# Kernel optimization log

Hardware: AMD Instinct MI355X
Metric: run time of the kernel (lower is better)

Reference implementation:

```python
import jax, jax.numpy as jnp
import numpy as np
from jax import lax

DWT_SCALE = 0.5
IDWT_SCALE = 1.0
PAD = 2  # (kernel_size-1)//2 for k=5


def haar_dwt(x, s):
    """x: [B,C,H,W] -> (ll, lh, hl, hh) each [B,C,H/2,W/2]. 2x2 Haar, scale s."""
    a = x[..., 0::2, 0::2]
    b = x[..., 0::2, 1::2]
    c = x[..., 1::2, 0::2]
    d = x[..., 1::2, 1::2]
    ll = s * (a + b + c + d)
    lh = s * (a + b - c - d)
    hl = s * (a - b + c - d)
    hh = s * (a - b - c + d)
    return ll, lh, hl, hh


def haar_idwt(ll, lh, hl, hh, s):
    """Inverse of haar_dwt when s_dwt * s_idwt_total = 0.5. Returns [B,C,2H,2W]."""
    a = s * (ll + lh + hl + hh)
    b = s * (ll + lh - hl - hh)
    c = s * (ll - lh + hl - hh)
    d = s * (ll - lh - hl + hh)
    B, C, H2, W2 = ll.shape
    top = jnp.stack([a, b], axis=-1).reshape(B, C, H2, 2 * W2)  # even rows
    bot = jnp.stack([c, d], axis=-1).reshape(B, C, H2, 2 * W2)  # odd rows
    return jnp.stack([top, bot], axis=-2).reshape(B, C, 2 * H2, 2 * W2)


def conv2d(x, w, pad):
    return lax.conv_general_dilated(
        x, w, window_strides=(1, 1), padding=[(pad, pad), (pad, pad)],
        dimension_numbers=("NCHW", "OIHW", "NCHW"))


def setup_inputs() -> dict:
    key = jax.random.key(0)
    kx, k0, k1, k2, kb = jax.random.split(key, 5)
    C, K = 64, 5
    x = jax.random.normal(kx, (8, C, 256, 256), dtype=jnp.float32)
    # kaiming_uniform-ish small init to keep 3-level recursion numerically tame
    scale = 0.02
    w0 = jax.random.normal(k0, (4 * C, 4 * C, K, K), dtype=jnp.float32) * scale
    w1 = jax.random.normal(k1, (4 * C, 4 * C, K, K), dtype=jnp.float32) * scale
    w2 = jax.random.normal(k2, (4 * C, 4 * C, K, K), dtype=jnp.float32) * scale
    bias = jax.random.normal(kb, (C,), dtype=jnp.float32) * 0.01
    return {"x": x, "w0": w0, "w1": w1, "w2": w2, "bias": bias}


def reference(x, w0, w1, w2, bias):
    weights = [w0, w1, w2]
    idwt_s = DWT_SCALE * IDWT_SCALE  # perfect reconstruction pair
    curr = x
    ll_levels, high_levels = [], []
    for w in weights:
        ll, lh, hl, hh = haar_dwt(curr, DWT_SCALE)
        curr = ll  # pre-conv LL feeds the next level
        B, C, H2, W2 = ll.shape
        stacked = jnp.stack([ll, lh, hl, hh], axis=2).reshape(B, 4 * C, H2, W2)
        y = conv2d(stacked, w, PAD)  # [B, 4*Co, H2, W2]
        y = y.reshape(B, -1, 4, H2, W2)
        ll_levels.append(y[:, :, 0])
        high_levels.append(y[:, :, 1:])
    next_ll = jnp.zeros_like(ll_levels[-1])
    for ll_t, h_t in zip(reversed(ll_levels), reversed(high_levels)):
        ll = ll_t + next_ll
        next_ll = haar_idwt(ll, h_t[:, :, 0], h_t[:, :, 1], h_t[:, :, 2], idwt_s)
    return next_ll + bias.reshape(1, -1, 1, 1)
```

## Files before the change

### kernel.cpp

```cpp
#include <hip/hip_runtime.h>


typedef unsigned short u16;
typedef __attribute__((ext_vector_type(8))) __bf16 bf16x8;
typedef __attribute__((ext_vector_type(4))) float f32x4;

__device__ __forceinline__ u16 f2bf(float f) {
  union { float f; unsigned u; } v; v.f = f;
  unsigned r = v.u + 0x7fffu + ((v.u >> 16) & 1u);
  return (u16)(r >> 16);
}
__device__ __forceinline__ float bf2f(u16 u) {
  union { unsigned u; float f; } v; v.u = ((unsigned)u) << 16;
  return v.f;
}

typedef const unsigned int __attribute__((address_space(1)))* gas1_t;
typedef unsigned int __attribute__((address_space(3)))* gas3_t;
__device__ __forceinline__ void gload16(const void* g, void* l) {
  __builtin_amdgcn_global_load_lds((gas1_t)g, (gas3_t)l, 16, 0, 0);
}

__global__ void k_wtrans(const float* __restrict__ w, u16* __restrict__ wb) {
  int co = blockIdx.x;
  int ci = threadIdx.x;
  const float* src = w + ((long)co * 256 + ci) * 25;
  float v[25];
#pragma unroll
  for (int tp = 0; tp < 25; ++tp) v[tp] = src[tp];
#pragma unroll
  for (int tp = 0; tp < 25; ++tp)
    wb[((long)tp * 256 + co) * 256 + ci] = f2bf(v[tp]);
}

__global__ void k_dwt(const float* __restrict__ in, u16* __restrict__ st,
                      float* __restrict__ ll, int B_, int H2, int W2) {
  int idx = blockIdx.x * blockDim.x + threadIdx.x;
  int W2h = W2 >> 1;
  int total = B_ * 64 * H2 * W2h;
  if (idx >= total) return;
  int w2h = idx % W2h; int t2 = idx / W2h;
  int h2 = t2 % H2; t2 /= H2;
  int c = t2 % 64; int b = t2 / 64;
  int w2 = w2h * 2;
  const float* r0 = in + (((long)(b * 64 + c) * (2 * H2) + 2 * h2) * (2 * W2)) + 2 * w2;
  const float* r1 = r0 + 2 * W2;
  float4 tp = *(const float4*)r0;
  float4 bt = *(const float4*)r1;
  float ll0 = 0.5f * (tp.x + tp.y + bt.x + bt.y);
  float lh0 = 0.5f * (tp.x + tp.y - bt.x - bt.y);
  float hl0 = 0.5f * (tp.x - tp.y + bt.x - bt.y);
  float hh0 = 0.5f * (tp.x - tp.y - bt.x + bt.y);
  float ll1 = 0.5f * (tp.z + tp.w + bt.z + bt.w);
  float lh1 = 0.5f * (tp.z + tp.w - bt.z - bt.w);
  float hl1 = 0.5f * (tp.z - tp.w + bt.z - bt.w);
  float hh1 = 0.5f * (tp.z - tp.w - bt.z + bt.w);
  long sbase = (((long)b * (H2 + 4) + (h2 + 2)) * (W2 + 4) + (w2 + 2)) * 256 + 4 * c;
  *(ushort4*)(st + sbase)       = make_ushort4(f2bf(ll0), f2bf(lh0), f2bf(hl0), f2bf(hh0));
  *(ushort4*)(st + sbase + 256) = make_ushort4(f2bf(ll1), f2bf(lh1), f2bf(hl1), f2bf(hh1));
  long lbase = (((long)(b * 64 + c) * H2) + h2) * W2 + w2;
  *(float2*)(ll + lbase) = make_float2(ll0, ll1);
}

__global__ __launch_bounds__(512, 1) void k_conv_p(
    const u16* __restrict__ st, const u16* __restrict__ wt, u16* __restrict__ y,
    int H2, int W2) {
  __shared__ __align__(16) char smem[147456];
  const int t = threadIdx.x;
  const int lane = t & 63;
  const int wv = t >> 6;
  const int wm = wv >> 2;
  const int wn = wv & 3;
  const int nwg = gridDim.x;
  const int bid = blockIdx.x;
  const int lb = (bid & 7) * (nwg >> 3) + (bid >> 3);
  const int m0 = lb * 128;
  const int PW = W2 + 4;

  const int trow = t >> 3;
  const int srcci = ((t & 7) ^ (trow & 7)) * 8;
  const char* baseA[2];
  const char* baseB[4];
#pragma unroll
  for (int h = 0; h < 2; ++h) {
    int m = m0 + h * 64 + trow;
    int w = m % W2; int q = m / W2;
    int hh = q % H2; int b = q / H2;
    long sp = ((long)(b * (H2 + 4) + hh + 2) * PW + (w + 2));
    baseA[h] = (const char*)(st + sp * 256 + srcci);
  }
#pragma unroll
  for (int u = 0; u < 4; ++u) {
    int n = u * 64 + trow;
    baseB[u] = (const char*)(wt + (long)n * 256 + srcci);
  }

  f32x4 acc[4][4];
#pragma unroll
  for (int i = 0; i < 4; ++i)
#pragma unroll
    for (int j = 0; j < 4; ++j) acc[i][j] = f32x4{0.f, 0.f, 0.f, 0.f};

  const int kq = (lane >> 4) * 16;
  int aoff[2][4], boff[2][4];
#pragma unroll
  for (int ks = 0; ks < 2; ++ks)
#pragma unroll
    for (int i = 0; i < 4; ++i) {
      int ra = wm * 64 + i * 16 + (lane & 15);
      int kb = ks * 64 + kq;
      aoff[ks][i] = ra * 128 + (kb ^ ((ra & 7) << 4));
      int rb = wn * 64 + i * 16 + (lane & 15);
      boff[ks][i] = 16384 + rb * 128 + (kb ^ ((rb & 7) << 4));
    }

  auto stage_a = [&](int kt) {
    int tap = kt >> 2, cic = kt & 3;
    int dy = tap / 5 - 2, dx = tap % 5 - 2;
    long offA = ((long)(dy * PW + dx) * 256 + cic * 64) * 2;
    long offB = ((long)tap * 65536 + cic * 64) * 2;
    char* lb2 = smem + (kt % 3) * 49152 + wv * 1024;
    gload16(baseA[0] + offA, lb2);
    gload16(baseA[1] + offA, lb2 + 8192);
    gload16(baseB[0] + offB, lb2 + 16384);
  };
  auto stage_b = [&](int kt) {
    int tap = kt >> 2, cic = kt & 3;
    long offB = ((long)tap * 65536 + cic * 64) * 2;
    char* lb2 = smem + (kt % 3) * 49152 + wv * 1024;
    gload16(baseB[1] + offB, lb2 + 24576);
    gload16(baseB[2] + offB, lb2 + 32768);
    gload16(baseB[3] + offB, lb2 + 40960);
  };

  stage_a(0); stage_b(0);
  stage_a(1); stage_b(1);
  asm volatile("s_waitcnt vmcnt(6)" ::: "memory");
  __builtin_amdgcn_s_barrier();

  for (int kt = 0; kt < 100; ++kt) {
    const char* la = smem + (kt % 3) * 49152;
    const bool st2 = (kt + 2) < 100;
    bf16x8 af[4], bfr[4];
#pragma unroll
    for (int i = 0; i < 4; ++i) af[i] = *(const bf16x8*)(la + aoff[0][i]);
#pragma unroll
    for (int j = 0; j < 4; ++j) bfr[j] = *(const bf16x8*)(la + boff[0][j]);
    if (st2) stage_a(kt + 2);
    __builtin_amdgcn_s_barrier();
    asm volatile("s_waitcnt lgkmcnt(0)" ::: "memory");
    __builtin_amdgcn_sched_barrier(0);
    __builtin_amdgcn_s_setprio(1);
#pragma unroll
    for (int i = 0; i < 4; ++i)
#pragma unroll
      for (int j = 0; j < 4; ++j)
        acc[i][j] = __builtin_amdgcn_mfma_f32_16x16x32_bf16(af[i], bfr[j], acc[i][j], 0, 0, 0);
    __builtin_amdgcn_s_setprio(0);
    __builtin_amdgcn_s_barrier();
#pragma unroll
    for (int i = 0; i < 4; ++i) af[i] = *(const bf16x8*)(la + aoff[1][i]);
#pragma unroll
    for (int j = 0; j < 4; ++j) bfr[j] = *(const bf16x8*)(la + boff[1][j]);
    if (st2) stage_b(kt + 2);
    __builtin_amdgcn_s_barrier();
    asm volatile("s_waitcnt lgkmcnt(0)" ::: "memory");
    __builtin_amdgcn_sched_barrier(0);
    __builtin_amdgcn_s_setprio(1);
#pragma unroll
    for (int i = 0; i < 4; ++i)
#pragma unroll
      for (int j = 0; j < 4; ++j)
        acc[i][j] = __builtin_amdgcn_mfma_f32_16x16x32_bf16(af[i], bfr[j], acc[i][j], 0, 0, 0);
    __builtin_amdgcn_s_setprio(0);
    if (st2) {
      asm volatile("s_waitcnt vmcnt(6)" ::: "memory");
    } else if (kt + 1 < 100) {
      asm volatile("s_waitcnt vmcnt(0)" ::: "memory");
    }
    __builtin_amdgcn_s_barrier();
  }

#pragma unroll
  for (int i = 0; i < 4; ++i) {
    int mloc = m0 + wm * 64 + i * 16 + (lane >> 4) * 4;
#pragma unroll
    for (int j = 0; j < 4; ++j) {
      int nloc = wn * 64 + j * 16 + (lane & 15);
#pragma unroll
      for (int r = 0; r < 4; ++r)
        y[(long)(mloc + r) * 256 + nloc] = f2bf(acc[i][j][r]);
    }
  }
}

__global__ __launch_bounds__(256) void k_conv(
    const u16* __restrict__ st, const u16* __restrict__ wt, u16* __restrict__ y,
    int H2, int W2) {
  __shared__ __align__(16) char smem[32768];
  const int t = threadIdx.x;
  const int lane = t & 63;
  const int wv = t >> 6;
  const int wm = wv >> 1, wn = wv & 1;
  const int m0 = blockIdx.x * 128;
  const int n0 = blockIdx.y * 128;
  const int PW = W2 + 4;
  const int lsub = lane & 7;
  const int lrow8 = lane >> 3;
  const int srcci = (lsub ^ lrow8) * 8;

  const char* baseA[4];
  const char* baseB[4];
#pragma unroll
  for (int l = 0; l < 4; ++l) {
    int ml = (wv * 4 + l) * 8 + lrow8;
    int m = m0 + ml;
    int w = m % W2;
    int q = m / W2;
    int h = q % H2;
    int b = q / H2;
    long sp = ((long)(b * (H2 + 4) + h + 2) * PW + (w + 2));
    baseA[l] = (const char*)(st + sp * 256 + srcci);
    int nl = n0 + (wv * 4 + l) * 8 + lrow8;
    baseB[l] = (const char*)(wt + (long)nl * 256 + srcci);
  }

  f32x4 acc[4][4];
#pragma unroll
  for (int i = 0; i < 4; ++i)
#pragma unroll
    for (int j = 0; j < 4; ++j) acc[i][j] = f32x4{0.f, 0.f, 0.f, 0.f};

  const int arow = wm * 64 + (lane & 15);
  const int brow = wn * 64 + (lane & 15);
  const int kq = (lane >> 4) * 16;
  int aoff[2][4], boff[2][4];
#pragma unroll
  for (int ks = 0; ks < 2; ++ks)
#pragma unroll
    for (int i = 0; i < 4; ++i) {
      int ra = arow + i * 16;
      int kb = ks * 64 + kq;
      aoff[ks][i] = ra * 128 + (kb ^ ((ra & 7) << 4));
      int rb = brow + i * 16;
      boff[ks][i] = 16384 + rb * 128 + (kb ^ ((rb & 7) << 4));
    }

  for (int kk = 0; kk < 100; ++kk) {
    const int tap = kk >> 2, cic = kk & 3;
    const int dy = tap / 5 - 2, dx = tap % 5 - 2;
    const int offA = ((dy * PW + dx) * 256 + cic * 64) * 2;
    const int offB = (tap * 65536 + cic * 64) * 2;
#pragma unroll
    for (int l = 0; l < 4; ++l) {
      gload16(baseA[l] + offA, smem + (wv * 4 + l) * 1024);
      gload16(baseB[l] + offB, smem + 16384 + (wv * 4 + l) * 1024);
    }
    __syncthreads();
#pragma unroll
    for (int ks = 0; ks < 2; ++ks) {
      bf16x8 af[4], bfr[4];
#pragma unroll
      for (int i = 0; i < 4; ++i) af[i] = *(const bf16x8*)(smem + aoff[ks][i]);
#pragma unroll
      for (int j = 0; j < 4; ++j) bfr[j] = *(const bf16x8*)(smem + boff[ks][j]);
#pragma unroll
      for (int i = 0; i < 4; ++i)
#pragma unroll
        for (int j = 0; j < 4; ++j)
          acc[i][j] = __builtin_amdgcn_mfma_f32_16x16x32_bf16(af[i], bfr[j], acc[i][j], 0, 0, 0);
    }
    __syncthreads();
  }

  const long ybase = (long)m0 * 256 + n0;
#pragma unroll
  for (int i = 0; i < 4; ++i) {
    int mloc = wm * 64 + i * 16 + (lane >> 4) * 4;
#pragma unroll
    for (int j = 0; j < 4; ++j) {
      int nloc = wn * 64 + j * 16 + (lane & 15);
#pragma unroll
      for (int r = 0; r < 4; ++r)
        y[ybase + (long)(mloc + r) * 256 + nloc] = f2bf(acc[i][j][r]);
    }
  }
}

__global__ void k_idwt(const u16* __restrict__ y, const float* __restrict__ nll,
                       float* __restrict__ out, const float* __restrict__ bias,
                       int B_, int H2, int W2) {
  int idx = blockIdx.x * blockDim.x + threadIdx.x;
  int W2h = W2 >> 1;
  int total = B_ * 64 * H2 * W2h;
  if (idx >= total) return;
  int w2h = idx % W2h; int t2 = idx / W2h;
  int h2 = t2 % H2; t2 /= H2;
  int c = t2 % 64; int b = t2 / 64;
  int w2 = w2h * 2;
  long ybase = (((long)b * H2 + h2) * W2 + w2) * 256 + 4 * c;
  ushort4 q0 = *(const ushort4*)(y + ybase);
  ushort4 q1 = *(const ushort4*)(y + ybase + 256);
  float llv0 = bf2f(q0.x), lh0 = bf2f(q0.y), hl0 = bf2f(q0.z), hh0 = bf2f(q0.w);
  float llv1 = bf2f(q1.x), lh1 = bf2f(q1.y), hl1 = bf2f(q1.z), hh1 = bf2f(q1.w);
  if (nll) {
    float2 nv = *(const float2*)(nll + (((long)(b * 64 + c) * H2 + h2) * W2 + w2));
    llv0 += nv.x; llv1 += nv.y;
  }
  float bv = bias ? bias[c] : 0.f;
  float a0 = 0.5f * (llv0 + lh0 + hl0 + hh0) + bv;
  float b0 = 0.5f * (llv0 + lh0 - hl0 - hh0) + bv;
  float c0 = 0.5f * (llv0 - lh0 + hl0 - hh0) + bv;
  float d0 = 0.5f * (llv0 - lh0 - hl0 + hh0) + bv;
  float a1 = 0.5f * (llv1 + lh1 + hl1 + hh1) + bv;
  float b1 = 0.5f * (llv1 + lh1 - hl1 - hh1) + bv;
  float c1 = 0.5f * (llv1 - lh1 + hl1 - hh1) + bv;
  float d1 = 0.5f * (llv1 - lh1 - hl1 + hh1) + bv;
  long obase = (((long)(b * 64 + c) * (2 * H2) + 2 * h2) * (2 * W2)) + 2 * w2;
  *(float4*)(out + obase)             = make_float4(a0, b0, a1, b1);
  *(float4*)(out + obase + 2 * W2)    = make_float4(c0, d0, c1, d1);
}

constexpr size_t WBF_SZ1 = 25ull * 256 * 256 * 2;
constexpr size_t OFF_WBF = 0;
constexpr size_t OFF_S0  = 3 * WBF_SZ1;
constexpr size_t S0_SZ   = 8ull * 132 * 132 * 256 * 2;
constexpr size_t REL_S1 = 0;
constexpr size_t S1_SZ  = 8ull * 68 * 68 * 256 * 2;
constexpr size_t REL_L1 = REL_S1 + S1_SZ;
constexpr size_t L1_SZ  = 8ull * 64 * 64 * 64 * 4;
constexpr size_t REL_S2 = REL_L1 + L1_SZ;
constexpr size_t S2_SZ  = 8ull * 36 * 36 * 256 * 2;
constexpr size_t REL_Y1 = REL_S2 + S2_SZ;
constexpr size_t Y1_SZ  = 8ull * 64 * 64 * 256 * 2;
constexpr size_t REL_Y2 = REL_Y1 + Y1_SZ;
constexpr size_t Y2_SZ  = 8ull * 32 * 32 * 256 * 2;
constexpr size_t REL_N2 = REL_Y2 + Y2_SZ;
constexpr size_t N2_SZ  = 8ull * 64 * 64 * 64 * 4;
constexpr size_t REL_L2 = REL_N2 + N2_SZ;
constexpr size_t OFF_L0 = OFF_S0 + S0_SZ;
constexpr size_t L0_SZ  = 8ull * 64 * 128 * 128 * 4;
constexpr size_t OFF_Y0 = OFF_L0 + L0_SZ;
constexpr size_t Y0_SZ  = 8ull * 128 * 128 * 256 * 2;

extern "C" void kernel_launch(void* const* d_in, const int* in_sizes, int n_in,
                              void* d_out, int out_size, void* d_ws, size_t ws_size,
                              hipStream_t stream) {
  const float* x    = (const float*)d_in[0];
  const float* w0   = (const float*)d_in[1];
  const float* w1   = (const float*)d_in[2];
  const float* w2   = (const float*)d_in[3];
  const float* bias = (const float*)d_in[4];
  float* out = (float*)d_out;
  char* ws = (char*)d_ws;

  u16* wbf0 = (u16*)(ws + OFF_WBF);
  u16* wbf1 = (u16*)(ws + OFF_WBF + WBF_SZ1);
  u16* wbf2 = (u16*)(ws + OFF_WBF + 2 * WBF_SZ1);
  u16* s0 = (u16*)(ws + OFF_S0);
  u16* s1 = (u16*)(ws + OFF_S0 + REL_S1);
  float* l1 = (float*)(ws + OFF_S0 + REL_L1);
  u16* s2 = (u16*)(ws + OFF_S0 + REL_S2);
  u16* y1 = (u16*)(ws + OFF_S0 + REL_Y1);
  u16* y2 = (u16*)(ws + OFF_S0 + REL_Y2);
  float* n2 = (float*)(ws + OFF_S0 + REL_N2);
  float* l2 = (float*)(ws + OFF_S0 + REL_L2);
  float* l0 = (float*)(ws + OFF_L0);
  float* n1 = (float*)(ws + OFF_L0);
  u16* y0 = (u16*)(ws + OFF_Y0);

  k_wtrans<<<256, 256, 0, stream>>>(w0, wbf0);
  k_wtrans<<<256, 256, 0, stream>>>(w1, wbf1);
  k_wtrans<<<256, 256, 0, stream>>>(w2, wbf2);

  (void)hipMemsetAsync(s0, 0, S0_SZ, stream);
  k_dwt<<<16384, 256, 0, stream>>>(x, s0, l0, 8, 128, 128);
  k_conv_p<<<1024, 512, 0, stream>>>(s0, wbf0, y0, 128, 128);

  (void)hipMemsetAsync(s1, 0, S1_SZ, stream);
  (void)hipMemsetAsync(s2, 0, S2_SZ, stream);

  k_dwt<<<4096, 256, 0, stream>>>(l0, s1, l1, 8, 64, 64);
  k_conv_p<<<256, 512, 0, stream>>>(s1, wbf1, y1, 64, 64);

  k_dwt<<<1024, 256, 0, stream>>>(l1, s2, l2, 8, 32, 32);
  k_conv<<<dim3(64, 2), 256, 0, stream>>>(s2, wbf2, y2, 32, 32);

  k_idwt<<<1024, 256, 0, stream>>>(y2, nullptr, n2, nullptr, 8, 32, 32);
  k_idwt<<<4096, 256, 0, stream>>>(y1, n2, n1, nullptr, 8, 64, 64);
  k_idwt<<<16384, 256, 0, stream>>>(y0, n1, out, bias, 8, 128, 128);
}
```

Before: 790.3 us.

## Use 256x256-tile implicit-GEMM conv for level 0 and zero only pad borders

Adds k_conv8, a level-0 convolution kernel with a 256-row M tile, an 8x4 MFMA accumulator per wave, double-buffered LDS and split A/B staging interleaved with four MFMA quarter-steps. Larger tiles raise operand reuse and halve the number of workgroups, cutting global and LDS traffic per FLOP. Separately, full hipMemset of the padded stacked buffers is replaced by a k_border kernel that zeroes only the 2-pixel halo, avoiding writes to the interior that k_dwt overwrites anyway. The bigger tile raises register pressure and leaves 512 workgroups, which may underfill or unevenly load the CUs.

```diff
diff --git a/kernel.cpp b/kernel.cpp
--- a/kernel.cpp
+++ b/kernel.cpp
@@ -31,6 +31,21 @@
 #pragma unroll
   for (int tp = 0; tp < 25; ++tp)
     wb[((long)tp * 256 + co) * 256 + ci] = f2bf(v[tp]);
+}
+
+__global__ void k_border(u16* __restrict__ st, int B_, int H2, int W2) {
+  int PW = W2 + 4;
+  int npix = 4 * PW + 4 * H2;
+  int gid = blockIdx.x * blockDim.x + threadIdx.x;
+  int pid = gid >> 6, lane = gid & 63;
+  if (pid >= B_ * npix) return;
+  int b = pid / npix, p = pid % npix;
+  int row, col;
+  if (p < 2 * PW) { row = p / PW; col = p % PW; }
+  else if (p < 4 * PW) { int q = p - 2 * PW; row = H2 + 2 + q / PW; col = q % PW; }
+  else { int q = p - 4 * PW; row = 2 + (q >> 2); int c4 = q & 3; col = (c4 < 2) ? c4 : W2 + c4; }
+  long base = (((long)b * (H2 + 4) + row) * PW + col) * 256 + lane * 4;
+  *(ushort4*)(st + base) = make_ushort4(0, 0, 0, 0);
 }
 
 __global__ void k_dwt(const float* __restrict__ in, u16* __restrict__ st,
@@ -62,6 +77,147 @@
   *(float2*)(ll + lbase) = make_float2(ll0, ll1);
 }
 
+__global__ __launch_bounds__(512, 1) void k_conv8(
+    const u16* __restrict__ st, const u16* __restrict__ wt, u16* __restrict__ y,
+    int H2, int W2) {
+  __shared__ __align__(16) char smem[131072];
+  const int t = threadIdx.x;
+  const int lane = t & 63;
+  const int wv = t >> 6;
+  const int wm = wv >> 2, wn = wv & 3;
+  const int nwg = gridDim.x;
+  const int bid = blockIdx.x;
+  const int lb = (bid & 7) * (nwg >> 3) + (bid >> 3);
+  const int m0 = lb * 256;
+  const int PW = W2 + 4;
+
+  const int trow = t >> 3;
+  const int srcci = ((t & 7) ^ (trow & 7)) * 8;
+  const char* baseA[4];
+#pragma unroll
+  for (int u = 0; u < 4; ++u) {
+    int m = m0 + u * 64 + trow;
+    int w = m % W2; int q = m / W2;
+    int hh = q % H2; int b = q / H2;
+    long sp = ((long)(b * (H2 + 4) + hh + 2) * PW + (w + 2));
+    baseA[u] = (const char*)(st + sp * 256 + srcci);
+  }
+  const char* baseB0 = (const char*)(wt + trow * 256 + srcci);
+
+  f32x4 acc[8][4];
+#pragma unroll
+  for (int i = 0; i < 8; ++i)
+#pragma unroll
+    for (int j = 0; j < 4; ++j) acc[i][j] = f32x4{0.f, 0.f, 0.f, 0.f};
+
+  const int kq = (lane >> 4) * 16;
+  const int sw = (lane & 7) << 4;
+  const int kx0 = (kq) ^ sw;
+  const int kx1 = (64 + kq) ^ sw;
+  const int aBase = (wm * 128 + (lane & 15)) * 128;
+  const int bBase = 32768 + (wn * 64 + (lane & 15)) * 128;
+
+  auto stageA = [&](int kt, char* dst, int up) {
+    int tap = kt >> 2, cic = kt & 3;
+    int dy = tap / 5 - 2, dx = tap % 5 - 2;
+    long off = ((long)(dy * PW + dx) * 256 + cic * 64) * 2;
+#pragma unroll
+    for (int u = up * 2; u < up * 2 + 2; ++u)
+      gload16(baseA[u] + off, dst + u * 8192 + wv * 1024);
+  };
+  auto stageB = [&](int kt, char* dst, int up) {
+    int tap = kt >> 2, cic = kt & 3;
+    long off = ((long)tap * 65536 + cic * 64) * 2;
+#pragma unroll
+    for (int u = up * 2; u < up * 2 + 2; ++u)
+      gload16(baseB0 + u * 32768 + off, dst + 32768 + u * 8192 + wv * 1024);
+  };
+
+#define QMFMA(mh, nh)                                                              \
+  _Pragma("unroll") for (int i = 0; i < 4; ++i)                                    \
+  _Pragma("unroll") for (int jj = 0; jj < 2; ++jj)                                 \
+  _Pragma("unroll") for (int ks = 0; ks < 2; ++ks)                                 \
+    acc[(mh)*4 + i][(nh)*2 + jj] = __builtin_amdgcn_mfma_f32_16x16x32_bf16(        \
+        af[mh][i][ks], bfr[jj][ks], acc[(mh)*4 + i][(nh)*2 + jj], 0, 0, 0);
+
+  stageA(0, smem, 0); stageA(0, smem, 1);
+  stageB(0, smem, 0); stageB(0, smem, 1);
+  stageA(1, smem + 65536, 0); stageA(1, smem + 65536, 1);
+  asm volatile("s_waitcnt vmcnt(4)" ::: "memory");
+  __builtin_amdgcn_s_barrier();
+
+  for (int kt = 0; kt < 100; ++kt) {
+    char* bufp = smem + (kt & 1) * 65536;
+    char* altp = smem + ((kt & 1) ^ 1) * 65536;
+    bf16x8 af[2][4][2], bfr[2][2];
+#pragma unroll
+    for (int i = 0; i < 4; ++i) {
+      af[0][i][0] = *(const bf16x8*)(bufp + aBase + i * 2048 + kx0);
+      af[0][i][1] = *(const bf16x8*)(bufp + aBase + i * 2048 + kx1);
+    }
+#pragma unroll
+    for (int jj = 0; jj < 2; ++jj) {
+      bfr[jj][0] = *(const bf16x8*)(bufp + bBase + jj * 2048 + kx0);
+      bfr[jj][1] = *(const bf16x8*)(bufp + bBase + jj * 2048 + kx1);
+    }
+    if (kt + 1 < 100) stageB(kt + 1, altp, 0);
+    __builtin_amdgcn_s_barrier();
+    asm volatile("s_waitcnt lgkmcnt(0)" ::: "memory");
+    __builtin_amdgcn_sched_barrier(0);
+    __builtin_amdgcn_s_setprio(1);
+    QMFMA(0, 0)
+    __builtin_amdgcn_s_setprio(0);
+    __builtin_amdgcn_s_barrier();
+#pragma unroll
+    for (int i = 0; i < 4; ++i) {
+      af[1][i][0] = *(const bf16x8*)(bufp + aBase + (4 + i) * 2048 + kx0);
+      af[1][i][1] = *(const bf16x8*)(bufp + aBase + (4 + i) * 2048 + kx1);
+    }
+    if (kt + 1 < 100) stageB(kt + 1, altp, 1);
+    __builtin_amdgcn_s_barrier();
+    asm volatile("s_waitcnt lgkmcnt(0)" ::: "memory");
+    __builtin_amdgcn_sched_barrier(0);
+    __builtin_amdgcn_s_setprio(1);
+    QMFMA(1, 0)
+    __builtin_amdgcn_s_setprio(0);
+    __builtin_amdgcn_s_barrier();
+#pragma unroll
+    for (int jj = 0; jj < 2; ++jj) {
+      bfr[jj][0] = *(const bf16x8*)(bufp + bBase + (2 + jj) * 2048 + kx0);
+      bfr[jj][1] = *(const bf16x8*)(bufp + bBase + (2 + jj) * 2048 + kx1);
+    }
+    if (kt + 2 < 100) stageA(kt + 2, bufp, 0);
+    __builtin_amdgcn_s_barrier();
+    asm volatile("s_waitcnt lgkmcnt(0)" ::: "memory");
+    __builtin_amdgcn_sched_barrier(0);
+    __builtin_amdgcn_s_setprio(1);
+    QMFMA(0, 1)
+    __builtin_amdgcn_s_setprio(0);
+    __builtin_amdgcn_s_barrier();
+    if (kt + 2 < 100) stageA(kt + 2, bufp, 1);
+    __builtin_amdgcn_s_barrier();
+    __builtin_amdgcn_s_setprio(1);
+    QMFMA(1, 1)
+    __builtin_amdgcn_s_setprio(0);
+    if (kt < 98) { asm volatile("s_waitcnt vmcnt(4)" ::: "memory"); }
+    else if (kt == 98) { asm volatile("s_waitcnt vmcnt(0)" ::: "memory"); }
+    __builtin_amdgcn_s_barrier();
+  }
+#undef QMFMA
+
+#pragma unroll
+  for (int i = 0; i < 8; ++i) {
+    int mloc = m0 + wm * 128 + i * 16 + (lane >> 4) * 4;
+#pragma unroll
+    for (int j = 0; j < 4; ++j) {
+      int nloc = wn * 64 + j * 16 + (lane & 15);
+#pragma unroll
+      for (int r = 0; r < 4; ++r)
+        y[(long)(mloc + r) * 256 + nloc] = f2bf(acc[i][j][r]);
+    }
+  }
+}
+
 __global__ __launch_bounds__(512, 1) void k_conv_p(
     const u16* __restrict__ st, const u16* __restrict__ wt, u16* __restrict__ y,
     int H2, int W2) {
@@ -317,8 +473,8 @@
   float c1 = 0.5f * (llv1 - lh1 + hl1 - hh1) + bv;
   float d1 = 0.5f * (llv1 - lh1 - hl1 + hh1) + bv;
   long obase = (((long)(b * 64 + c) * (2 * H2) + 2 * h2) * (2 * W2)) + 2 * w2;
-  *(float4*)(out + obase)             = make_float4(a0, b0, a1, b1);
-  *(float4*)(out + obase + 2 * W2)    = make_float4(c0, d0, c1, d1);
+  *(float4*)(out + obase)          = make_float4(a0, b0, a1, b1);
+  *(float4*)(out + obase + 2 * W2) = make_float4(c0, d0, c1, d1);
 }
 
 constexpr size_t WBF_SZ1 = 25ull * 256 * 256 * 2;
@@ -373,12 +529,12 @@
   k_wtrans<<<256, 256, 0, stream>>>(w1, wbf1);
   k_wtrans<<<256, 256, 0, stream>>>(w2, wbf2);
 
-  (void)hipMemsetAsync(s0, 0, S0_SZ, stream);
+  k_border<<<2080, 256, 0, stream>>>(s0, 8, 128, 128);
   k_dwt<<<16384, 256, 0, stream>>>(x, s0, l0, 8, 128, 128);
-  k_conv_p<<<1024, 512, 0, stream>>>(s0, wbf0, y0, 128, 128);
-
-  (void)hipMemsetAsync(s1, 0, S1_SZ, stream);
-  (void)hipMemsetAsync(s2, 0, S2_SZ, stream);
+  k_conv8<<<512, 512, 0, stream>>>(s0, wbf0, y0, 128, 128);
+
+  k_border<<<1056, 256, 0, stream>>>(s1, 8, 64, 64);
+  k_border<<<544, 256, 0, stream>>>(s2, 8, 32, 32);
 
   k_dwt<<<4096, 256, 0, stream>>>(l0, s1, l1, 8, 64, 64);
   k_conv_p<<<256, 512, 0, stream>>>(s1, wbf1, y1, 64, 64);
```

Result: faster. 741.6 us (-6.2%).
